# Optimization experiments

Measured on AMD Instinct MI355X. Metric: run time of the kernel, lower is better.

## Reference

```python
import jax, jax.numpy as jnp
import numpy as np

N = 4096          # batch of candidate observations
D = 1024          # embedding dim
N_CLASSES = 100
GTG_MAX_ITER = 30 # gtg_tol=0.0 -> while loop always runs max_iter steps
PERC_LABELED = 0.5
EPS = 1e-8        # matches the +1e-08 in sum_X_A_X


def setup_inputs() -> dict:
    key = jax.random.key(0)
    k1, k2 = jax.random.split(key)
    embedding = jax.random.normal(k1, (N, D), dtype=jnp.float32)
    labels = jax.random.randint(k2, (N,), 0, N_CLASSES, dtype=jnp.int32)
    return {"embedding": embedding, "labels": labels}


def _cos_affinity(E):
    # F.normalize(E, dim=-1) with eps=1e-12, then relu(En @ En.T), diag := 1
    En = E / jnp.maximum(jnp.linalg.norm(E, axis=-1, keepdims=True), 1e-12)
    A = jax.nn.relu(En @ En.T)                      # [N, N]
    n = A.shape[0]
    idx = jnp.arange(n)
    A = A.at[idx, idx].set(1.0)
    return A, En


def reference(embedding, labels):
    n = embedding.shape[0]

    # ---- get_A_rbfk (A_function='cos_sim', rbf_aff=True) ----
    A, En = _cos_affinity(embedding)
    # 7th neighbor by descending cosine similarity (column index 6)
    idx7 = jnp.argsort(-A, axis=1)[:, 6]            # [N]
    # sigma_i = relu(cos(x_i, seventh_i)) -- the [0,1] entry of the 2x2 cos-sim matrix
    sigmas = jax.nn.relu(jnp.sum(En * En[idx7], axis=-1))  # [N]
    A = jnp.exp(-(A ** 2) / (sigmas[:, None] * sigmas[None, :]))

    # ---- threshold (strategy='mean', cos_sim branch) ----
    A = jnp.where(A < jnp.mean(A), 0.0, A)

    # ---- get_X: first n_lab indices labeled (one-hot), rest uniform 1/C ----
    n_lab = int(n * PERC_LABELED)
    labeled = jnp.arange(n) < n_lab                 # [N] bool
    one_hot = jax.nn.one_hot(labels, N_CLASSES, dtype=jnp.float32)
    X0 = jnp.where(labeled[:, None], one_hot, jnp.float32(1.0 / N_CLASSES))

    # ---- graph transduction game: X <- (X + X*(A@X)) / rowsum ----
    def step(X, _):
        mm_A_X = A @ X                              # [N, C]
        mult = X + X * mm_A_X
        Xn = mult / (jnp.sum(mult, axis=1, keepdims=True) + EPS)
        ent = -jnp.sum(Xn * jnp.log(Xn + EPS), axis=1)  # per-row entropy history
        return Xn, ent

    Xf, _ent_hist = jax.lax.scan(step, X0, None, length=GTG_MAX_ITER)
    return Xf
```

## Files before the change

kernel.cpp:

```cpp
#include <hip/hip_runtime.h>
#include <math.h>

typedef unsigned short ushortT;
typedef __attribute__((ext_vector_type(8))) short short8;
typedef __attribute__((ext_vector_type(4))) float f32x4;

#define NN 4096
#define DD 1024
#define NC 100
#define CP 128
#define NLAB 2048
#define NITER 30

__device__ __forceinline__ ushortT bf16rn(float x) {
  unsigned u = __float_as_uint(x);
  unsigned r = (u + 0x7fffu + ((u >> 16) & 1u)) >> 16;
  return (ushortT)r;
}
__device__ __forceinline__ float bf2f(ushortT h) {
  return __uint_as_float(((unsigned)h) << 16);
}
__device__ __forceinline__ void gload16(const void* g, void* l) {
  __builtin_amdgcn_global_load_lds((const __attribute__((address_space(1))) char*)g,
                                   (__attribute__((address_space(3))) char*)l, 16, 0, 0);
}

__global__ __launch_bounds__(256) void k_normalize(const float* __restrict__ E,
                                                   ushortT* __restrict__ Enh,
                                                   ushortT* __restrict__ Enl) {
  int row = blockIdx.x, t = threadIdx.x;
  const float4* e4 = (const float4*)(E + (size_t)row * DD);
  float4 v = e4[t];
  float ss = v.x * v.x + v.y * v.y + v.z * v.z + v.w * v.w;
  __shared__ float red[4];
  int lane = t & 63, w = t >> 6;
#pragma unroll
  for (int off = 32; off; off >>= 1) ss += __shfl_xor(ss, off);
  if (lane == 0) red[w] = ss;
  __syncthreads();
  float tot = red[0] + red[1] + red[2] + red[3];
  float d = fmaxf(sqrtf(tot), 1e-12f);
  float xs[4] = {v.x / d, v.y / d, v.z / d, v.w / d};
  ushort4 hv, lv;
  ushortT h;
  h = bf16rn(xs[0]); hv.x = h; lv.x = bf16rn(xs[0] - bf2f(h));
  h = bf16rn(xs[1]); hv.y = h; lv.y = bf16rn(xs[1] - bf2f(h));
  h = bf16rn(xs[2]); hv.z = h; lv.z = bf16rn(xs[2] - bf2f(h));
  h = bf16rn(xs[3]); hv.w = h; lv.w = bf16rn(xs[3] - bf2f(h));
  ((ushort4*)Enh)[(size_t)row * 256 + t] = hv;
  ((ushort4*)Enl)[(size_t)row * 256 + t] = lv;
}

__global__ __launch_bounds__(256, 4) void k_syrk_mfma(const ushortT* __restrict__ Enh,
                                                      const ushortT* __restrict__ Enl,
                                                      float* __restrict__ A) {
  int xg = (int)blockIdx.x & 7;
  int j = (int)blockIdx.x >> 3;
  int bi = -1, bj = 0;
#pragma unroll
  for (int p = 0; p < 4; ++p) {
    int bic = xg + (p << 3);
    int c = 32 - bic;
    if (bi < 0) {
      if (j < c) { bi = bic; bj = bic + j; } else j -= c;
    }
  }
  if (bi < 0) return;
  __shared__ ushortT lds[18432];
  int t = threadIdx.x;
  int l = t & 63, w = t >> 6;
  int i0 = bi << 7, j0 = bj << 7;
  int wr = w >> 1, wc = w & 1;
  f32x4 zz = {0.f, 0.f, 0.f, 0.f};
  f32x4 acc[4][4];
#pragma unroll
  for (int m = 0; m < 4; ++m)
#pragma unroll
    for (int n = 0; n < 4; ++n) acc[m][n] = zz;
  int arow_l = l & 15, kslot = l >> 4;

  for (int s = 0; s < 48; ++s) {
    int term = s >> 4;
    int kk0 = (s & 15) << 6;
    const ushortT* sa = (term == 2) ? Enl : Enh;
    const ushortT* sb = (term == 1) ? Enl : Enh;
#pragma unroll
    for (int q = 0; q < 4; ++q) {
      int n = (q << 8) + t;
      int r = n >> 3, p = n & 7;
      int col = (p ^ (r & 7)) << 3;
      gload16(sa + (size_t)(i0 + r) * DD + kk0 + col, &lds[n << 3]);
      gload16(sb + (size_t)(j0 + r) * DD + kk0 + col, &lds[8192 + (n << 3)]);
    }
    __syncthreads();
#pragma unroll
    for (int kk = 0; kk < 2; ++kk) {
      int g = (kk << 2) + kslot;
      short8 av[4], bv[4];
#pragma unroll
      for (int m = 0; m < 4; ++m) {
        int r = (wr << 6) + (m << 4) + arow_l;
        av[m] = *(const short8*)&lds[(r << 6) + ((g ^ (r & 7)) << 3)];
      }
#pragma unroll
      for (int n = 0; n < 4; ++n) {
        int r = (wc << 6) + (n << 4) + arow_l;
        bv[n] = *(const short8*)&lds[8192 + (r << 6) + ((g ^ (r & 7)) << 3)];
      }
#pragma unroll
      for (int m = 0; m < 4; ++m)
#pragma unroll
        for (int n = 0; n < 4; ++n)
          acc[m][n] = __builtin_amdgcn_mfma_f32_16x16x32_bf16(av[m], bv[n], acc[m][n], 0, 0, 0);
    }
    __syncthreads();
  }
  int rbase = (l >> 4) << 2;
#pragma unroll
  for (int m = 0; m < 4; ++m) {
#pragma unroll
    for (int n = 0; n < 4; ++n) {
#pragma unroll
      for (int r = 0; r < 4; ++r) {
        int gi = i0 + (wr << 6) + (m << 4) + rbase + r;
        int gj = j0 + (wc << 6) + (n << 4) + (l & 15);
        float v = fmaxf(acc[m][n][r], 0.0f);
        if (gi == gj) v = 1.0f;
        A[(size_t)gi * NN + gj] = v;
      }
    }
  }
  if (bi != bj) {
    float* T = (float*)&lds[0];
#pragma unroll
    for (int c2 = 0; c2 < 2; ++c2) {
      __syncthreads();
      if (wr == c2) {
#pragma unroll
        for (int m = 0; m < 4; ++m)
#pragma unroll
          for (int n = 0; n < 4; ++n)
#pragma unroll
            for (int r = 0; r < 4; ++r)
              T[(((wc << 6) + (n << 4) + (l & 15)) * 68) + (m << 4) + rbase + r] =
                  fmaxf(acc[m][n][r], 0.0f);
      }
      __syncthreads();
      int lj = t >> 1, cg = (t & 1) << 5;
#pragma unroll
      for (int q = 0; q < 8; ++q) {
        float4 vq = *(const float4*)&T[lj * 68 + cg + (q << 2)];
        *(float4*)&A[(size_t)(j0 + lj) * NN + i0 + (c2 << 6) + cg + (q << 2)] = vq;
      }
    }
  }
}

__device__ __forceinline__ void ins7(float (&tv)[7], float v) {
  if (v > tv[6]) {
#pragma unroll
    for (int s = 0; s < 7; s++) {
      if (v > tv[s]) { float tmp = tv[s]; tv[s] = v; v = tmp; }
    }
  }
}
__global__ __launch_bounds__(256) void k_top7(const float* __restrict__ A,
                                              float* __restrict__ sig) {
  int w = threadIdx.x >> 6, lane = threadIdx.x & 63;
  int row = (blockIdx.x << 2) + w;
  const float4* a4 = (const float4*)(A + (size_t)row * NN);
  float tv[7];
#pragma unroll
  for (int i = 0; i < 7; i++) tv[i] = -1.0f;
  for (int k = 0; k < 16; k++) {
    float4 v = a4[(k << 6) + lane];
    ins7(tv, v.x); ins7(tv, v.y); ins7(tv, v.z); ins7(tv, v.w);
  }
  int head = 0;
  float seventh = 0.0f;
  for (int r = 0; r < 7; r++) {
    float h = (head < 7) ? tv[head] : -1.0f;
    float m = h;
#pragma unroll
    for (int off = 32; off; off >>= 1) m = fmaxf(m, __shfl_xor(m, off));
    unsigned long long ball = __ballot(h == m);
    if (lane == (__ffsll(ball) - 1)) head++;
    seventh = m;
  }
  if (lane == 0) sig[row] = seventh;
}

__global__ __launch_bounds__(256) void k_transform(const float* __restrict__ A,
                                                   const float* __restrict__ sig,
                                                   double* __restrict__ parts) {
  int row = blockIdx.x;
  float si = sig[row];
  const float4* a4 = (const float4*)(A + (size_t)row * NN);
  const float4* s4 = (const float4*)sig;
  int t = threadIdx.x;
  double local = 0.0;
#pragma unroll
  for (int k = 0; k < 4; k++) {
    int j = (k << 8) + t;
    float4 v = a4[j];
    float4 sg = s4[j];
    local += (double)expf(-(v.x * v.x) / (si * sg.x)) +
             (double)expf(-(v.y * v.y) / (si * sg.y)) +
             (double)expf(-(v.z * v.z) / (si * sg.z)) +
             (double)expf(-(v.w * v.w) / (si * sg.w));
  }
  __shared__ double dred[4];
  int lane = t & 63, wv = t >> 6;
#pragma unroll
  for (int off = 32; off; off >>= 1) local += __shfl_xor(local, off);
  if (lane == 0) dred[wv] = local;
  __syncthreads();
  if (t == 0) parts[row] = dred[0] + dred[1] + dred[2] + dred[3];
}

__global__ __launch_bounds__(256) void k_mean(const double* __restrict__ parts,
                                              float* __restrict__ meanb) {
  int t = threadIdx.x;
  double local = 0.0;
#pragma unroll
  for (int k = 0; k < NN / 256; k++) local += parts[(k << 8) + t];
  __shared__ double dred[4];
  int lane = t & 63, wv = t >> 6;
#pragma unroll
  for (int off = 32; off; off >>= 1) local += __shfl_xor(local, off);
  if (lane == 0) dred[wv] = local;
  __syncthreads();
  if (t == 0) meanb[0] = (float)((dred[0] + dred[1] + dred[2] + dred[3]) / ((double)NN * (double)NN));
}

__global__ __launch_bounds__(256) void k_thresh_pack(const float* __restrict__ A,
                                                     const float* __restrict__ sig,
                                                     const float* __restrict__ meanb,
                                                     ushortT* __restrict__ ApL,
                                                     ushortT* __restrict__ ApU) {
  float m = meanb[0];
  int i4 = ((int)blockIdx.x << 8) + threadIdx.x;
  int row2 = i4 >> 10;
  int col4 = (i4 & 1023) << 2;
  int grow = NLAB + row2;
  float si = sig[grow];
  float4 v = *(const float4*)&A[(size_t)grow * NN + col4];
  float4 sg = *(const float4*)&sig[col4];
  float c0 = expf(-(v.x * v.x) / (si * sg.x));
  float c1 = expf(-(v.y * v.y) / (si * sg.y));
  float c2 = expf(-(v.z * v.z) / (si * sg.z));
  float c3 = expf(-(v.w * v.w) / (si * sg.w));
  c0 = (c0 < m) ? 0.0f : c0;
  c1 = (c1 < m) ? 0.0f : c1;
  c2 = (c2 < m) ? 0.0f : c2;
  c3 = (c3 < m) ? 0.0f : c3;
  int half = col4 >> 11;
  int cc = col4 & 2047;
  int rt = row2 >> 4, arow = row2 & 15;
  int kc = cc >> 5, khi = (cc >> 3) & 3, k0 = cc & 7;
  ushortT* dst = half ? ApU : ApL;
  ushort4 hv;
  hv.x = bf16rn(c0); hv.y = bf16rn(c1); hv.z = bf16rn(c2); hv.w = bf16rn(c3);
  *(ushort4*)&dst[((size_t)((rt << 6) + kc) << 9) + (khi << 7) + (arow << 3) + k0] = hv;
}

__global__ __launch_bounds__(256) void k_xlabp(const int* __restrict__ labels,
                                               ushortT* __restrict__ Xlabp) {
  int idx = ((int)blockIdx.x << 8) + threadIdx.x;
  int c = idx >> 11, j = idx & 2047;
  int kc = j >> 5, khi = (j >> 3) & 3, k0 = j & 7;
  int cf = c >> 4, slot = c & 15;
  Xlabp[((size_t)(((kc << 3) + cf) << 2) + khi) * 128 + (slot << 3) + k0] =
      (labels[j] == c) ? (ushortT)0x3F80 : (ushortT)0;
}

__global__ __launch_bounds__(64) void k_xinit(float* __restrict__ Xf,
                                              ushortT* __restrict__ Xp) {
  int rt = blockIdx.x, l = threadIdx.x;
  int col = l & 15, rg4 = l >> 4;
  int kc = rt >> 1;
  int kk = ((rt & 1) << 4) + (rg4 << 2);
  int khi = kk >> 3, k0 = kk & 7;
#pragma unroll
  for (int cf = 0; cf < 8; ++cf) {
    int cls = (cf << 4) + col;
    float v = (cls < NC) ? 0.01f : 0.0f;
    ((f32x4*)Xf)[(size_t)((rt << 3) + cf) * 64 + l] = (f32x4){v, v, v, v};
    ushortT h = bf16rn(v);
    ushort4 hv = {h, h, h, h};
    *(ushort4*)&Xp[((size_t)(((kc << 3) + cf) << 2) + khi) * 128 + (col << 3) + k0] = hv;
  }
}

__global__ __launch_bounds__(256) void k_gP(const ushortT* __restrict__ Ap,
                                            const ushortT* __restrict__ Xp,
                                            float* __restrict__ Pp) {
  int t = threadIdx.x, l = t & 63, w = t >> 6;
  int bid = (int)blockIdx.x;
  int rt = ((bid & 7) << 4) + ((bid >> 3) & 15);
  int s = bid >> 7;
  int kc0 = (s << 4) + (w << 2);
  const ushortT* ab = Ap + ((size_t)rt << 15) + ((size_t)kc0 << 9) + (l << 3);
  const ushortT* xb = Xp + ((size_t)kc0 << 12) + (l << 3);
  short8 av[4];
#pragma unroll
  for (int i = 0; i < 4; ++i) av[i] = *(const short8*)(ab + ((size_t)i << 9));
  f32x4 acc[8];
#pragma unroll
  for (int cf = 0; cf < 8; ++cf) {
    acc[cf] = (f32x4){0.f, 0.f, 0.f, 0.f};
#pragma unroll
    for (int i = 0; i < 4; ++i) {
      short8 bv = *(const short8*)(xb + ((size_t)i << 12) + (cf << 9));
      acc[cf] = __builtin_amdgcn_mfma_f32_16x16x32_bf16(av[i], bv, acc[cf], 0, 0, 0);
    }
  }
  __shared__ float red[4][8][64][4];
#pragma unroll
  for (int cf = 0; cf < 8; ++cf) *(f32x4*)&red[w][cf][l][0] = acc[cf];
  __syncthreads();
  if (w < 2) {
#pragma unroll
    for (int q = 0; q < 4; ++q) {
      int cf = (w << 2) + q;
      f32x4 sum = *(const f32x4*)&red[0][cf][l][0];
#pragma unroll
      for (int wp = 1; wp < 4; ++wp) {
        f32x4 p = *(const f32x4*)&red[wp][cf][l][0];
        sum[0] += p[0]; sum[1] += p[1]; sum[2] += p[2]; sum[3] += p[3];
      }
      ((f32x4*)Pp)[((size_t)(((s << 7) + rt) << 3) + cf) * 64 + l] = sum;
    }
  }
}

__global__ __launch_bounds__(64) void k_updY(const float* __restrict__ Pp,
                                             float* __restrict__ YlabF) {
  int rt = blockIdx.x, l = threadIdx.x;
#pragma unroll
  for (int cf = 0; cf < 8; ++cf) {
    f32x4 acc = (f32x4){0.f, 0.f, 0.f, 0.f};
#pragma unroll
    for (int s = 0; s < 4; ++s) {
      f32x4 p = ((const f32x4*)Pp)[((size_t)(((s << 7) + rt) << 3) + cf) * 64 + l];
      acc[0] += p[0]; acc[1] += p[1]; acc[2] += p[2]; acc[3] += p[3];
    }
    ((f32x4*)YlabF)[(size_t)((rt << 3) + cf) * 64 + l] = acc;
  }
}

__global__ __launch_bounds__(256) void k_it2(
    const ushortT* __restrict__ Ap,
    const ushortT* __restrict__ Xp,
    const float* __restrict__ YlabF, const float* __restrict__ XfPrev,
    float* __restrict__ XfOut, ushortT* __restrict__ XpOut,
    float* __restrict__ sums2,
    int* __restrict__ cnt2) {
  __shared__ float red[4][4][64][4];
  __shared__ float sums_l[4][16];
  __shared__ float totl[16];
  int t = threadIdx.x, l = t & 63, w = t >> 6;
  int bid = (int)blockIdx.x;
  int rt = ((bid & 7) << 4) + ((bid >> 3) & 15);
  int half = bid >> 7;
  int cf = (half << 2) + w;

  const ushortT* ab = Ap + ((size_t)rt << 15) + ((size_t)(w << 4) << 9) + (l << 3);
  const ushortT* xb = Xp + ((size_t)(w << 4) << 12) + ((size_t)(half << 2) << 9) + (l << 3);
  f32x4 acc[4];
#pragma unroll
  for (int cc = 0; cc < 4; ++cc) acc[cc] = (f32x4){0.f, 0.f, 0.f, 0.f};
#pragma unroll
  for (int i = 0; i < 16; ++i) {
    short8 av = *(const short8*)(ab + ((size_t)i << 9));
#pragma unroll
    for (int cc = 0; cc < 4; ++cc) {
      short8 bv = *(const short8*)(xb + ((size_t)i << 12) + (cc << 9));
      acc[cc] = __builtin_amdgcn_mfma_f32_16x16x32_bf16(av, bv, acc[cc], 0, 0, 0);
    }
  }
#pragma unroll
  for (int cc = 0; cc < 4; ++cc) *(f32x4*)&red[w][cc][l][0] = acc[cc];
  __syncthreads();
  f32x4 mm = (f32x4){0.f, 0.f, 0.f, 0.f};
#pragma unroll
  for (int wp = 0; wp < 4; ++wp) {
    f32x4 p = *(const f32x4*)&red[wp][w][l][0];
    mm[0] += p[0]; mm[1] += p[1]; mm[2] += p[2]; mm[3] += p[3];
  }
  size_t fo = (size_t)((rt << 3) + cf) * 64 + l;
  f32x4 yl = ((const f32x4*)YlabF)[fo];
  f32x4 xv = ((const f32x4*)XfPrev)[fo];
  f32x4 mult, rs;
#pragma unroll
  for (int r = 0; r < 4; ++r) {
    mult[r] = fmaf(xv[r], mm[r] + yl[r], xv[r]);
    rs[r] = mult[r];
  }
#pragma unroll
  for (int msk = 1; msk < 16; msk <<= 1) {
#pragma unroll
    for (int r = 0; r < 4; ++r) rs[r] += __shfl_xor(rs[r], msk);
  }
  int rg4 = l >> 4, col16 = l & 15;
  if (col16 == 0) {
#pragma unroll
    for (int r = 0; r < 4; ++r) sums_l[w][(rg4 << 2) + r] = rs[r];
  }
  __syncthreads();
  if (w == 0 && l < 16) {
    float hs = sums_l[0][l] + sums_l[1][l] + sums_l[2][l] + sums_l[3][l];
    atomicAdd(&sums2[(rt << 4) + l], hs);
  }
  if (t == 0) {
    asm volatile("s_waitcnt vmcnt(0)" ::: "memory");
    atomicAdd(&cnt2[rt], 1);
    while (atomicAdd(&cnt2[rt], 0) < 2) __builtin_amdgcn_s_sleep(2);
  }
  __syncthreads();
  if (w == 0 && l < 16) totl[l] = atomicAdd(&sums2[(rt << 4) + l], 0.0f) + 1e-8f;
  __syncthreads();
  f32x4 ov;
#pragma unroll
  for (int r = 0; r < 4; ++r) ov[r] = mult[r] / totl[(rg4 << 2) + r];
  ((f32x4*)XfOut)[fo] = ov;
  int kcp = rt >> 1;
  int rem = ((rt & 1) << 4) + (rg4 << 2);
  int khi = rem >> 3, k0 = rem & 7;
  ushort4 xo;
  xo.x = bf16rn(ov[0]); xo.y = bf16rn(ov[1]);
  xo.z = bf16rn(ov[2]); xo.w = bf16rn(ov[3]);
  *(ushort4*)&XpOut[((size_t)(((kcp << 3) + cf) << 2) + khi) * 128 + (col16 << 3) + k0] = xo;
}

__global__ __launch_bounds__(256) void k_output(const float* __restrict__ Xf,
                                                const int* __restrict__ labels,
                                                float* __restrict__ out) {
  int idx = ((int)blockIdx.x << 8) + threadIdx.x;
  int i = idx / NC, c = idx - i * NC;
  float v;
  if (i < NLAB) {
    v = (labels[i] == c) ? 1.0f : 0.0f;
  } else {
    int row = i - NLAB;
    int rt = row >> 4, r = row & 15;
    int rg4 = r >> 2, reg = r & 3;
    int cf = c >> 4, col = c & 15;
    v = Xf[((size_t)(((rt << 3) + cf) << 6) + (rg4 << 4) + col) * 4 + reg];
  }
  out[idx] = v;
}

extern "C" void kernel_launch(void* const* d_in, const int* in_sizes, int n_in,
                              void* d_out, int out_size, void* d_ws, size_t ws_size,
                              hipStream_t stream) {
  const float* E = (const float*)d_in[0];
  const int* labels = (const int*)d_in[1];
  float* out = (float*)d_out;
  char* ws = (char*)d_ws;
  const size_t MB = 1024 * 1024;

  float* A = (float*)ws;
  ushortT* Enh = (ushortT*)(ws + 64 * MB);
  ushortT* Enl = (ushortT*)(ws + 72 * MB);
  ushortT* ApL = (ushortT*)(ws + 80 * MB);
  ushortT* ApU = (ushortT*)(ws + 88 * MB);
  float* sig = (float*)(ws + 96 * MB);
  double* parts = (double*)(ws + 96 * MB + 65536);
  float* meanb = (float*)(ws + 96 * MB + 131072);
  ushortT* Xlabp = (ushortT*)(ws + 97 * MB);
  float* YlabF = (float*)(ws + 98 * MB);
  float* Xf0 = (float*)(ws + 99 * MB);
  float* Xf1 = (float*)(ws + 100 * MB);
  ushortT* Xp0 = (ushortT*)(ws + 101 * MB);
  ushortT* Xp1 = (ushortT*)(ws + 102 * MB);
  float* Pp = (float*)(ws + 104 * MB);
  float* sums2 = (float*)(ws + 108 * MB);
  int* cnt2 = (int*)(ws + 109 * MB);

  k_normalize<<<NN, 256, 0, stream>>>(E, Enh, Enl);
  k_syrk_mfma<<<640, 256, 0, stream>>>(Enh, Enl, A);
  k_top7<<<NN / 4, 256, 0, stream>>>(A, sig);
  k_transform<<<NN, 256, 0, stream>>>(A, sig, parts);
  k_mean<<<1, 256, 0, stream>>>(parts, meanb);
  k_thresh_pack<<<8192, 256, 0, stream>>>(A, sig, meanb, ApL, ApU);
  k_xlabp<<<1024, 256, 0, stream>>>(labels, Xlabp);
  k_xinit<<<128, 64, 0, stream>>>(Xf0, Xp0);
  hipMemsetAsync(sums2, 0, (size_t)NITER * 128 * 16 * sizeof(float), stream);
  hipMemsetAsync(cnt2, 0, (size_t)NITER * 128 * sizeof(int), stream);
  k_gP<<<512, 256, 0, stream>>>(ApL, Xlabp, Pp);
  k_updY<<<128, 64, 0, stream>>>(Pp, YlabF);
  float* xf[2] = {Xf0, Xf1};
  ushortT* xp[2] = {Xp0, Xp1};
  int cur = 0;
  for (int it = 0; it < NITER; ++it) {
    int nxt = cur ^ 1;
    k_it2<<<256, 256, 0, stream>>>(ApU, xp[cur], YlabF, xf[cur], xf[nxt], xp[nxt],
                                   sums2 + (size_t)it * 2048, cnt2 + (size_t)it * 128);
    cur = nxt;
  }
  k_output<<<1600, 256, 0, stream>>>(xf[cur], labels, out);
}
```

Measured before the change: 478.4 us.

## Drop split-bf16 Gram matrix and store cosine affinity as bf16

Replaces the three-term hi/lo bf16 compensated GEMM with a single bf16 product, cutting the MFMA and load work of the Gram matrix by a factor of three. The affinity matrix A is now stored as bf16 instead of fp32, halving its write and the reads in top7, transform and threshold-pack, which are retuned for 8-wide loads. The cost is lower precision in the cosine similarities, which feed the 7th-neighbor selection, sigma, the mean threshold and the GTG iterations, so the output may drift from the fp32 reference.

```diff
diff --git a/kernel.cpp b/kernel.cpp
--- a/kernel.cpp
+++ b/kernel.cpp
@@ -26,8 +26,7 @@
 }
 
 __global__ __launch_bounds__(256) void k_normalize(const float* __restrict__ E,
-                                                   ushortT* __restrict__ Enh,
-                                                   ushortT* __restrict__ Enl) {
+                                                   ushortT* __restrict__ Enh) {
   int row = blockIdx.x, t = threadIdx.x;
   const float4* e4 = (const float4*)(E + (size_t)row * DD);
   float4 v = e4[t];
@@ -40,20 +39,14 @@
   __syncthreads();
   float tot = red[0] + red[1] + red[2] + red[3];
   float d = fmaxf(sqrtf(tot), 1e-12f);
-  float xs[4] = {v.x / d, v.y / d, v.z / d, v.w / d};
-  ushort4 hv, lv;
-  ushortT h;
-  h = bf16rn(xs[0]); hv.x = h; lv.x = bf16rn(xs[0] - bf2f(h));
-  h = bf16rn(xs[1]); hv.y = h; lv.y = bf16rn(xs[1] - bf2f(h));
-  h = bf16rn(xs[2]); hv.z = h; lv.z = bf16rn(xs[2] - bf2f(h));
-  h = bf16rn(xs[3]); hv.w = h; lv.w = bf16rn(xs[3] - bf2f(h));
+  ushort4 hv;
+  hv.x = bf16rn(v.x / d); hv.y = bf16rn(v.y / d);
+  hv.z = bf16rn(v.z / d); hv.w = bf16rn(v.w / d);
   ((ushort4*)Enh)[(size_t)row * 256 + t] = hv;
-  ((ushort4*)Enl)[(size_t)row * 256 + t] = lv;
 }
 
 __global__ __launch_bounds__(256, 4) void k_syrk_mfma(const ushortT* __restrict__ Enh,
-                                                      const ushortT* __restrict__ Enl,
-                                                      float* __restrict__ A) {
+                                                      ushortT* __restrict__ A) {
   int xg = (int)blockIdx.x & 7;
   int j = (int)blockIdx.x >> 3;
   int bi = -1, bj = 0;
@@ -79,18 +72,15 @@
     for (int n = 0; n < 4; ++n) acc[m][n] = zz;
   int arow_l = l & 15, kslot = l >> 4;
 
-  for (int s = 0; s < 48; ++s) {
-    int term = s >> 4;
-    int kk0 = (s & 15) << 6;
-    const ushortT* sa = (term == 2) ? Enl : Enh;
-    const ushortT* sb = (term == 1) ? Enl : Enh;
+  for (int s = 0; s < 16; ++s) {
+    int kk0 = s << 6;
 #pragma unroll
     for (int q = 0; q < 4; ++q) {
       int n = (q << 8) + t;
       int r = n >> 3, p = n & 7;
       int col = (p ^ (r & 7)) << 3;
-      gload16(sa + (size_t)(i0 + r) * DD + kk0 + col, &lds[n << 3]);
-      gload16(sb + (size_t)(j0 + r) * DD + kk0 + col, &lds[8192 + (n << 3)]);
+      gload16(Enh + (size_t)(i0 + r) * DD + kk0 + col, &lds[n << 3]);
+      gload16(Enh + (size_t)(j0 + r) * DD + kk0 + col, &lds[8192 + (n << 3)]);
     }
     __syncthreads();
 #pragma unroll
@@ -126,7 +116,7 @@
         int gj = j0 + (wc << 6) + (n << 4) + (l & 15);
         float v = fmaxf(acc[m][n][r], 0.0f);
         if (gi == gj) v = 1.0f;
-        A[(size_t)gi * NN + gj] = v;
+        A[(size_t)gi * NN + gj] = bf16rn(v);
       }
     }
   }
@@ -148,9 +138,15 @@
       __syncthreads();
       int lj = t >> 1, cg = (t & 1) << 5;
 #pragma unroll
-      for (int q = 0; q < 8; ++q) {
-        float4 vq = *(const float4*)&T[lj * 68 + cg + (q << 2)];
-        *(float4*)&A[(size_t)(j0 + lj) * NN + i0 + (c2 << 6) + cg + (q << 2)] = vq;
+      for (int q = 0; q < 4; ++q) {
+        float4 a0 = *(const float4*)&T[lj * 68 + cg + (q << 3)];
+        float4 a1 = *(const float4*)&T[lj * 68 + cg + (q << 3) + 4];
+        short8 o;
+        o[0] = (short)bf16rn(a0.x); o[1] = (short)bf16rn(a0.y);
+        o[2] = (short)bf16rn(a0.z); o[3] = (short)bf16rn(a0.w);
+        o[4] = (short)bf16rn(a1.x); o[5] = (short)bf16rn(a1.y);
+        o[6] = (short)bf16rn(a1.z); o[7] = (short)bf16rn(a1.w);
+        *(short8*)&A[(size_t)(j0 + lj) * NN + i0 + (c2 << 6) + cg + (q << 3)] = o;
       }
     }
   }
@@ -164,17 +160,19 @@
     }
   }
 }
-__global__ __launch_bounds__(256) void k_top7(const float* __restrict__ A,
+__global__ __launch_bounds__(256) void k_top7(const ushortT* __restrict__ A,
                                               float* __restrict__ sig) {
   int w = threadIdx.x >> 6, lane = threadIdx.x & 63;
   int row = (blockIdx.x << 2) + w;
-  const float4* a4 = (const float4*)(A + (size_t)row * NN);
+  const ushortT* a = A + (size_t)row * NN;
   float tv[7];
 #pragma unroll
   for (int i = 0; i < 7; i++) tv[i] = -1.0f;
-  for (int k = 0; k < 16; k++) {
-    float4 v = a4[(k << 6) + lane];
-    ins7(tv, v.x); ins7(tv, v.y); ins7(tv, v.z); ins7(tv, v.w);
+#pragma unroll
+  for (int k = 0; k < 8; k++) {
+    short8 v = *(const short8*)(a + (k << 9) + (lane << 3));
+#pragma unroll
+    for (int jj = 0; jj < 8; jj++) ins7(tv, bf2f((ushortT)v[jj]));
   }
   int head = 0;
   float seventh = 0.0f;
@@ -190,24 +188,30 @@
   if (lane == 0) sig[row] = seventh;
 }
 
-__global__ __launch_bounds__(256) void k_transform(const float* __restrict__ A,
+__global__ __launch_bounds__(256) void k_transform(const ushortT* __restrict__ A,
                                                    const float* __restrict__ sig,
                                                    double* __restrict__ parts) {
   int row = blockIdx.x;
   float si = sig[row];
-  const float4* a4 = (const float4*)(A + (size_t)row * NN);
-  const float4* s4 = (const float4*)sig;
+  const ushortT* a = A + (size_t)row * NN;
   int t = threadIdx.x;
   double local = 0.0;
 #pragma unroll
-  for (int k = 0; k < 4; k++) {
-    int j = (k << 8) + t;
-    float4 v = a4[j];
-    float4 sg = s4[j];
-    local += (double)expf(-(v.x * v.x) / (si * sg.x)) +
-             (double)expf(-(v.y * v.y) / (si * sg.y)) +
-             (double)expf(-(v.z * v.z) / (si * sg.z)) +
-             (double)expf(-(v.w * v.w) / (si * sg.w));
+  for (int k = 0; k < 2; k++) {
+    int idx = (k << 11) + (t << 3);
+    short8 v = *(const short8*)(a + idx);
+#pragma unroll
+    for (int q = 0; q < 2; ++q) {
+      float4 sg = *(const float4*)&sig[idx + (q << 2)];
+      float s0 = bf2f((ushortT)v[(q << 2) + 0]);
+      float s1 = bf2f((ushortT)v[(q << 2) + 1]);
+      float s2 = bf2f((ushortT)v[(q << 2) + 2]);
+      float s3 = bf2f((ushortT)v[(q << 2) + 3]);
+      local += (double)expf(-(s0 * s0) / (si * sg.x)) +
+               (double)expf(-(s1 * s1) / (si * sg.y)) +
+               (double)expf(-(s2 * s2) / (si * sg.z)) +
+               (double)expf(-(s3 * s3) / (si * sg.w));
+    }
   }
   __shared__ double dred[4];
   int lane = t & 63, wv = t >> 6;
@@ -233,35 +237,41 @@
   if (t == 0) meanb[0] = (float)((dred[0] + dred[1] + dred[2] + dred[3]) / ((double)NN * (double)NN));
 }
 
-__global__ __launch_bounds__(256) void k_thresh_pack(const float* __restrict__ A,
+__global__ __launch_bounds__(256) void k_thresh_pack(const ushortT* __restrict__ A,
                                                      const float* __restrict__ sig,
                                                      const float* __restrict__ meanb,
                                                      ushortT* __restrict__ ApL,
                                                      ushortT* __restrict__ ApU) {
   float m = meanb[0];
-  int i4 = ((int)blockIdx.x << 8) + threadIdx.x;
-  int row2 = i4 >> 10;
-  int col4 = (i4 & 1023) << 2;
+  int i8 = ((int)blockIdx.x << 8) + threadIdx.x;
+  int row2 = i8 >> 9;
+  int col8 = (i8 & 511) << 3;
   int grow = NLAB + row2;
   float si = sig[grow];
-  float4 v = *(const float4*)&A[(size_t)grow * NN + col4];
-  float4 sg = *(const float4*)&sig[col4];
-  float c0 = expf(-(v.x * v.x) / (si * sg.x));
-  float c1 = expf(-(v.y * v.y) / (si * sg.y));
-  float c2 = expf(-(v.z * v.z) / (si * sg.z));
-  float c3 = expf(-(v.w * v.w) / (si * sg.w));
-  c0 = (c0 < m) ? 0.0f : c0;
-  c1 = (c1 < m) ? 0.0f : c1;
-  c2 = (c2 < m) ? 0.0f : c2;
-  c3 = (c3 < m) ? 0.0f : c3;
-  int half = col4 >> 11;
-  int cc = col4 & 2047;
+  short8 v = *(const short8*)&A[(size_t)grow * NN + col8];
+  short8 o;
+#pragma unroll
+  for (int q = 0; q < 2; ++q) {
+    float4 sg = *(const float4*)&sig[col8 + (q << 2)];
+    float s0 = bf2f((ushortT)v[(q << 2) + 0]);
+    float s1 = bf2f((ushortT)v[(q << 2) + 1]);
+    float s2 = bf2f((ushortT)v[(q << 2) + 2]);
+    float s3 = bf2f((ushortT)v[(q << 2) + 3]);
+    float c0 = expf(-(s0 * s0) / (si * sg.x));
+    float c1 = expf(-(s1 * s1) / (si * sg.y));
+    float c2 = expf(-(s2 * s2) / (si * sg.z));
+    float c3 = expf(-(s3 * s3) / (si * sg.w));
+    o[(q << 2) + 0] = (short)((c0 < m) ? 0 : bf16rn(c0));
+    o[(q << 2) + 1] = (short)((c1 < m) ? 0 : bf16rn(c1));
+    o[(q << 2) + 2] = (short)((c2 < m) ? 0 : bf16rn(c2));
+    o[(q << 2) + 3] = (short)((c3 < m) ? 0 : bf16rn(c3));
+  }
+  int half = col8 >> 11;
+  int cc = col8 & 2047;
   int rt = row2 >> 4, arow = row2 & 15;
-  int kc = cc >> 5, khi = (cc >> 3) & 3, k0 = cc & 7;
+  int kc = cc >> 5, khi = (cc >> 3) & 3;
   ushortT* dst = half ? ApU : ApL;
-  ushort4 hv;
-  hv.x = bf16rn(c0); hv.y = bf16rn(c1); hv.z = bf16rn(c2); hv.w = bf16rn(c3);
-  *(ushort4*)&dst[((size_t)((rt << 6) + kc) << 9) + (khi << 7) + (arow << 3) + k0] = hv;
+  *(short8*)&dst[((size_t)((rt << 6) + kc) << 9) + (khi << 7) + (arow << 3)] = o;
 }
 
 __global__ __launch_bounds__(256) void k_xlabp(const int* __restrict__ labels,
@@ -350,12 +360,10 @@
 }
 
 __global__ __launch_bounds__(256) void k_it2(
-    const ushortT* __restrict__ Ap,
-    const ushortT* __restrict__ Xp,
+    const ushortT* __restrict__ Ap, const ushortT* __restrict__ Xp,
     const float* __restrict__ YlabF, const float* __restrict__ XfPrev,
     float* __restrict__ XfOut, ushortT* __restrict__ XpOut,
-    float* __restrict__ sums2,
-    int* __restrict__ cnt2) {
+    float* __restrict__ sums2, int* __restrict__ cnt2) {
   __shared__ float red[4][4][64][4];
   __shared__ float sums_l[4][16];
   __shared__ float totl[16];
@@ -460,30 +468,29 @@
   char* ws = (char*)d_ws;
   const size_t MB = 1024 * 1024;
 
-  float* A = (float*)ws;
-  ushortT* Enh = (ushortT*)(ws + 64 * MB);
-  ushortT* Enl = (ushortT*)(ws + 72 * MB);
-  ushortT* ApL = (ushortT*)(ws + 80 * MB);
-  ushortT* ApU = (ushortT*)(ws + 88 * MB);
-  float* sig = (float*)(ws + 96 * MB);
-  double* parts = (double*)(ws + 96 * MB + 65536);
-  float* meanb = (float*)(ws + 96 * MB + 131072);
-  ushortT* Xlabp = (ushortT*)(ws + 97 * MB);
-  float* YlabF = (float*)(ws + 98 * MB);
-  float* Xf0 = (float*)(ws + 99 * MB);
-  float* Xf1 = (float*)(ws + 100 * MB);
-  ushortT* Xp0 = (ushortT*)(ws + 101 * MB);
-  ushortT* Xp1 = (ushortT*)(ws + 102 * MB);
-  float* Pp = (float*)(ws + 104 * MB);
-  float* sums2 = (float*)(ws + 108 * MB);
-  int* cnt2 = (int*)(ws + 109 * MB);
-
-  k_normalize<<<NN, 256, 0, stream>>>(E, Enh, Enl);
-  k_syrk_mfma<<<640, 256, 0, stream>>>(Enh, Enl, A);
+  ushortT* A = (ushortT*)ws;
+  ushortT* Enh = (ushortT*)(ws + 32 * MB);
+  ushortT* ApL = (ushortT*)(ws + 40 * MB);
+  ushortT* ApU = (ushortT*)(ws + 48 * MB);
+  float* sig = (float*)(ws + 56 * MB);
+  double* parts = (double*)(ws + 56 * MB + 65536);
+  float* meanb = (float*)(ws + 56 * MB + 131072);
+  ushortT* Xlabp = (ushortT*)(ws + 57 * MB);
+  float* YlabF = (float*)(ws + 58 * MB);
+  float* Xf0 = (float*)(ws + 59 * MB);
+  float* Xf1 = (float*)(ws + 60 * MB);
+  ushortT* Xp0 = (ushortT*)(ws + 61 * MB);
+  ushortT* Xp1 = (ushortT*)(ws + 62 * MB);
+  float* Pp = (float*)(ws + 64 * MB);
+  float* sums2 = (float*)(ws + 68 * MB);
+  int* cnt2 = (int*)(ws + 69 * MB);
+
+  k_normalize<<<NN, 256, 0, stream>>>(E, Enh);
+  k_syrk_mfma<<<640, 256, 0, stream>>>(Enh, A);
   k_top7<<<NN / 4, 256, 0, stream>>>(A, sig);
   k_transform<<<NN, 256, 0, stream>>>(A, sig, parts);
   k_mean<<<1, 256, 0, stream>>>(parts, meanb);
-  k_thresh_pack<<<8192, 256, 0, stream>>>(A, sig, meanb, ApL, ApU);
+  k_thresh_pack<<<4096, 256, 0, stream>>>(A, sig, meanb, ApL, ApU);
   k_xlabp<<<1024, 256, 0, stream>>>(labels, Xlabp);
   k_xinit<<<128, 64, 0, stream>>>(Xf0, Xp0);
   hipMemsetAsync(sums2, 0, (size_t)NITER * 128 * 16 * sizeof(float), stream);
```

Result: faster. 428.8 us (-10.4%).
